# Kernel optimization log

Hardware: AMD Instinct MI355X
Metric: run time of the kernel (lower is better)

Reference implementation:

```python
import jax, jax.numpy as jnp
import numpy as np

D_MODEL = 1024
NUM_HEADS = 16
D_K = D_MODEL // NUM_HEADS


def setup_inputs() -> dict:
    key = jax.random.key(0)
    ks = jax.random.split(key, 11)
    B, T = 4, 2048
    s = 1.0 / np.sqrt(D_MODEL)
    inp = {
        'query': jax.random.normal(ks[0], (B, T, D_MODEL), jnp.float32),
        'key': jax.random.normal(ks[1], (B, T, D_MODEL), jnp.float32),
        'value': jax.random.normal(ks[2], (B, T, D_MODEL), jnp.float32),
        'Wq': jax.random.normal(ks[3], (D_MODEL, D_MODEL), jnp.float32) * s,
        'bq': jnp.zeros((D_MODEL,), jnp.float32),
        'Wk': jax.random.normal(ks[4], (D_MODEL, D_MODEL), jnp.float32) * s,
        'bk': jnp.zeros((D_MODEL,), jnp.float32),
        'Wv': jax.random.normal(ks[5], (D_MODEL, D_MODEL), jnp.float32) * s,
        'bv': jnp.zeros((D_MODEL,), jnp.float32),
        'Wo': jax.random.normal(ks[6], (D_MODEL, D_MODEL), jnp.float32) * s,
        'bo': jnp.zeros((D_MODEL,), jnp.float32),
    }
    return inp


def reference(query, key, value, Wq, bq, Wk, bk, Wv, bv, Wo, bo):
    B, Tq, _ = query.shape
    Tk = key.shape[1]
    # projections then split heads: [B,T,H,Dk] -> [B,H,T,Dk]
    Q = (query @ Wq + bq).reshape(B, Tq, NUM_HEADS, D_K).transpose(0, 2, 1, 3)
    K = (key @ Wk + bk).reshape(B, Tk, NUM_HEADS, D_K).transpose(0, 2, 1, 3)
    V = (value @ Wv + bv).reshape(B, Tk, NUM_HEADS, D_K).transpose(0, 2, 1, 3)
    scores = jnp.einsum('bhtd,bhsd->bhts', Q, K) / jnp.sqrt(jnp.float32(D_K))
    attn = jax.nn.softmax(scores, axis=-1)  # mask=None, dropout=0 (eval)
    ctx = jnp.einsum('bhts,bhsd->bhtd', attn, V)
    ctx = ctx.transpose(0, 2, 1, 3).reshape(B, Tq, D_MODEL)
    return ctx @ Wo + bo
```

## Files before the change

kernel.cpp:

```cpp
#include <hip/hip_runtime.h>
#include <hip/hip_bf16.h>
#include <stdint.h>

#define TSEQ 2048
#define NH   16
#define DKH  64
#define DM   1024

typedef __attribute__((ext_vector_type(8))) __bf16 bf16x8;
typedef __attribute__((ext_vector_type(4))) float floatx4;

#if __has_builtin(__builtin_amdgcn_exp2f)
#define EXP2F(x) __builtin_amdgcn_exp2f(x)
#else
#define EXP2F(x) exp2f(x)
#endif

__device__ __forceinline__ unsigned short f2bf(float f) {
  union { float f; unsigned u; } v; v.f = f;
  return (unsigned short)((v.u + 0x7fffu + ((v.u >> 16) & 1u)) >> 16);
}
__device__ __forceinline__ unsigned pack2bf(float a, float b) {
  float2 f; f.x = a; f.y = b;
  __hip_bfloat162 h = __float22bfloat162_rn(f);
  unsigned u; __builtin_memcpy(&u, &h, 4); return u;
}
__device__ __forceinline__ bf16x8 ld_frag(const unsigned short* p) {
  bf16x8 r; __builtin_memcpy(&r, p, 16); return r;
}
__device__ __forceinline__ void cp16(unsigned short* dst, const unsigned short* src) {
  uint4 t; __builtin_memcpy(&t, src, 16); __builtin_memcpy(dst, &t, 16);
}
__device__ __forceinline__ void cvt4(unsigned short* dst, const float* src) {
  float4 t; __builtin_memcpy(&t, src, 16);
  uint2 u; u.x = pack2bf(t.x, t.y); u.y = pack2bf(t.z, t.w);
  __builtin_memcpy(dst, &u, 8);
}

__global__ void wt_transpose(const float* __restrict__ in,
                             unsigned short* __restrict__ out) {
  __shared__ unsigned short tile[32][33];
  int bx = blockIdx.x * 32, by = blockIdx.y * 32;
  int x = threadIdx.x;
  for (int j = threadIdx.y; j < 32; j += 8)
    tile[j][x] = f2bf(in[(size_t)(by + j) * DM + bx + x]);
  __syncthreads();
  for (int j = threadIdx.y; j < 32; j += 8)
    out[(size_t)(bx + j) * DM + by + x] = tile[x][j];
}

template<int MODE>
__global__ __launch_bounds__(256, 2) void gemm_proj(
    const void* __restrict__ Araw,
    const unsigned short* __restrict__ WT,
    const float* __restrict__ bias,
    void* __restrict__ outraw) {
  const int LD = 40;
  __shared__ __align__(16) unsigned short Asm[128 * LD];
  __shared__ __align__(16) unsigned short Bsm[128 * LD];
  const int tid = threadIdx.x;
  const int wave = tid >> 6, lane = tid & 63;
  const int quad = lane >> 4, l16 = lane & 15;
  const int wm = wave & 1, wn = wave >> 1;
  const int m0 = blockIdx.y * 128, n0 = blockIdx.x * 128;

  floatx4 acc[4][4];
#pragma unroll
  for (int i = 0; i < 4; i++)
#pragma unroll
    for (int j = 0; j < 4; j++) acc[i][j] = (floatx4){0.f, 0.f, 0.f, 0.f};

  for (int k0 = 0; k0 < DM; k0 += 32) {
    if (MODE == 2) {
      const unsigned short* A16 = (const unsigned short*)Araw;
#pragma unroll
      for (int i = 0; i < 2; i++) {
        int c = tid + 256 * i;
        int row = c >> 2, k8 = (c & 3) * 8;
        cp16(&Asm[row * LD + k8], &A16[(size_t)(m0 + row) * DM + k0 + k8]);
      }
    } else {
      const float* A32 = (const float*)Araw;
#pragma unroll
      for (int i = 0; i < 4; i++) {
        int c = tid + 256 * i;
        int row = c >> 3, f4 = (c & 7) * 4;
        cvt4(&Asm[row * LD + f4], &A32[(size_t)(m0 + row) * DM + k0 + f4]);
      }
    }
#pragma unroll
    for (int i = 0; i < 2; i++) {
      int c = tid + 256 * i;
      int row = c >> 2, k8 = (c & 3) * 8;
      cp16(&Bsm[row * LD + k8], &WT[(size_t)(n0 + row) * DM + k0 + k8]);
    }
    __syncthreads();
    bf16x8 af[4], bfr[4];
#pragma unroll
    for (int mt = 0; mt < 4; mt++)
      af[mt] = ld_frag(&Asm[(wm * 64 + mt * 16 + l16) * LD + quad * 8]);
#pragma unroll
    for (int nt = 0; nt < 4; nt++)
      bfr[nt] = ld_frag(&Bsm[(wn * 64 + nt * 16 + l16) * LD + quad * 8]);
#pragma unroll
    for (int mt = 0; mt < 4; mt++)
#pragma unroll
      for (int nt = 0; nt < 4; nt++)
        acc[mt][nt] = __builtin_amdgcn_mfma_f32_16x16x32_bf16(af[mt], bfr[nt], acc[mt][nt], 0, 0, 0);
    __syncthreads();
  }

#pragma unroll
  for (int nt = 0; nt < 4; nt++) {
    int n = n0 + wn * 64 + nt * 16 + l16;
    float bv = bias[n];
#pragma unroll
    for (int mt = 0; mt < 4; mt++) {
#pragma unroll
      for (int r = 0; r < 4; r++) {
        int m = m0 + wm * 64 + mt * 16 + quad * 4 + r;
        float val = acc[mt][nt][r] + bv;
        if (MODE == 0) {
          int b = m >> 11, t = m & 2047, h = n >> 6, dk = n & 63;
          ((unsigned short*)outraw)[(size_t)(((b * NH + h) * TSEQ) + t) * DKH + dk] = f2bf(val);
        } else if (MODE == 1) {
          int b = m >> 11, t = m & 2047, h = n >> 6, dk = n & 63;
          ((unsigned short*)outraw)[(size_t)(((b * NH + h) * DKH) + dk) * TSEQ + t] = f2bf(val);
        } else {
          ((float*)outraw)[(size_t)m * DM + n] = val;
        }
      }
    }
  }
}

__global__ __launch_bounds__(256, 4) void flash_attn(
    const unsigned short* __restrict__ Q,
    const unsigned short* __restrict__ K,
    const unsigned short* __restrict__ VT,
    unsigned short* __restrict__ ctx) {
  const int LD = 72;
  __shared__ __align__(16) unsigned short QP[128 * LD];
  __shared__ __align__(16) unsigned short Ksm[64 * LD];
  __shared__ __align__(16) unsigned short Vsm[64 * LD];

  const int tid = threadIdx.x;
  const int wave = tid >> 6, lane = tid & 63;
  const int quad = lane >> 4, l16 = lane & 15;
  const int bh = blockIdx.y;
  const int t0 = blockIdx.x * 128;
  const unsigned short* Qg = Q + (size_t)bh * TSEQ * DKH;
  const unsigned short* Kg = K + (size_t)bh * TSEQ * DKH;
  const unsigned short* Vg = VT + (size_t)bh * DKH * TSEQ;

#pragma unroll
  for (int i = 0; i < 4; i++) {
    int c = tid + 256 * i;
    int row = c >> 3, k8 = (c & 7) * 8;
    cp16(&QP[row * LD + k8], &Qg[(size_t)(t0 + row) * DKH + k8]);
  }
  __syncthreads();
  bf16x8 qf[2][2];
#pragma unroll
  for (int qt = 0; qt < 2; qt++)
#pragma unroll
    for (int ks = 0; ks < 2; ks++)
      qf[qt][ks] = ld_frag(&QP[(wave * 32 + qt * 16 + l16) * LD + ks * 32 + quad * 8]);

  unsigned short* Pw = &QP[wave * 32 * LD];

  floatx4 O[2][4];
  float mrun[2], lrun[2];
#pragma unroll
  for (int qt = 0; qt < 2; qt++) {
#pragma unroll
    for (int dt = 0; dt < 4; dt++) O[qt][dt] = (floatx4){0.f, 0.f, 0.f, 0.f};
    mrun[qt] = -1e30f; lrun[qt] = 0.f;
  }
  const float sl = 0.125f * 1.44269504f;

  for (int j0 = 0; j0 < TSEQ; j0 += 64) {
#pragma unroll
    for (int i = 0; i < 2; i++) {
      int c = tid + 256 * i;
      int row = c >> 3, k8 = (c & 7) * 8;
      cp16(&Ksm[row * LD + k8], &Kg[(size_t)(j0 + row) * DKH + k8]);
      cp16(&Vsm[row * LD + k8], &Vg[(size_t)row * TSEQ + j0 + k8]);
    }
    __syncthreads();

    bf16x8 kf[4][2];
#pragma unroll
    for (int kt = 0; kt < 4; kt++)
#pragma unroll
      for (int ks = 0; ks < 2; ks++)
        kf[kt][ks] = ld_frag(&Ksm[(kt * 16 + l16) * LD + ks * 32 + quad * 8]);
    floatx4 st[4][2];
#pragma unroll
    for (int kt = 0; kt < 4; kt++)
#pragma unroll
      for (int qt = 0; qt < 2; qt++) {
        floatx4 a = (floatx4){0.f, 0.f, 0.f, 0.f};
        a = __builtin_amdgcn_mfma_f32_16x16x32_bf16(kf[kt][0], qf[qt][0], a, 0, 0, 0);
        a = __builtin_amdgcn_mfma_f32_16x16x32_bf16(kf[kt][1], qf[qt][1], a, 0, 0, 0);
        st[kt][qt] = a;
      }

    float aO[2][4];
#pragma unroll
    for (int qt = 0; qt < 2; qt++) {
      float mx = -3e38f;
#pragma unroll
      for (int kt = 0; kt < 4; kt++)
#pragma unroll
        for (int r = 0; r < 4; r++) mx = fmaxf(mx, st[kt][qt][r]);
      mx = fmaxf(mx, __shfl_xor(mx, 16, 64));
      mx = fmaxf(mx, __shfl_xor(mx, 32, 64));
      mx *= sl;
      float mnew = fmaxf(mrun[qt], mx);
      float alpha = EXP2F(mrun[qt] - mnew);
      mrun[qt] = mnew;
      float rs = 0.f;
#pragma unroll
      for (int kt = 0; kt < 4; kt++) {
        float p0 = EXP2F(st[kt][qt][0] * sl - mnew);
        float p1 = EXP2F(st[kt][qt][1] * sl - mnew);
        float p2 = EXP2F(st[kt][qt][2] * sl - mnew);
        float p3 = EXP2F(st[kt][qt][3] * sl - mnew);
        rs += (p0 + p1) + (p2 + p3);
        uint2 u; u.x = pack2bf(p0, p1); u.y = pack2bf(p2, p3);
        __builtin_memcpy(&Pw[(qt * 16 + l16) * LD + kt * 16 + quad * 4], &u, 8);
      }
      rs += __shfl_xor(rs, 16, 64);
      rs += __shfl_xor(rs, 32, 64);
      lrun[qt] = lrun[qt] * alpha + rs;
#pragma unroll
      for (int r = 0; r < 4; r++)
        aO[qt][r] = __shfl(alpha, quad * 20 + r, 64);
    }
    __syncthreads();

#pragma unroll
    for (int qt = 0; qt < 2; qt++)
#pragma unroll
      for (int dt = 0; dt < 4; dt++)
#pragma unroll
        for (int r = 0; r < 4; r++) O[qt][dt][r] *= aO[qt][r];

    bf16x8 vf[4][2];
#pragma unroll
    for (int dt = 0; dt < 4; dt++)
#pragma unroll
      for (int ks = 0; ks < 2; ks++)
        vf[dt][ks] = ld_frag(&Vsm[(dt * 16 + l16) * LD + ks * 32 + quad * 8]);
#pragma unroll
    for (int qt = 0; qt < 2; qt++) {
      bf16x8 pf[2];
#pragma unroll
      for (int ks = 0; ks < 2; ks++)
        pf[ks] = ld_frag(&Pw[(qt * 16 + l16) * LD + ks * 32 + quad * 8]);
#pragma unroll
      for (int dt = 0; dt < 4; dt++) {
        O[qt][dt] = __builtin_amdgcn_mfma_f32_16x16x32_bf16(pf[0], vf[dt][0], O[qt][dt], 0, 0, 0);
        O[qt][dt] = __builtin_amdgcn_mfma_f32_16x16x32_bf16(pf[1], vf[dt][1], O[qt][dt], 0, 0, 0);
      }
    }
    __syncthreads();
  }

  int b = bh >> 4, h = bh & 15;
#pragma unroll
  for (int qt = 0; qt < 2; qt++) {
#pragma unroll
    for (int r = 0; r < 4; r++) {
      float linv = 1.0f / __shfl(lrun[qt], quad * 20 + r, 64);
      int t = t0 + wave * 32 + qt * 16 + quad * 4 + r;
#pragma unroll
      for (int dt = 0; dt < 4; dt++) {
        int dk = dt * 16 + l16;
        ctx[((size_t)b * TSEQ + t) * DM + h * DKH + dk] = f2bf(O[qt][dt][r] * linv);
      }
    }
  }
}

extern "C" void kernel_launch(void* const* d_in, const int* in_sizes, int n_in,
                              void* d_out, int out_size, void* d_ws, size_t ws_size,
                              hipStream_t stream) {
  const float* q  = (const float*)d_in[0];
  const float* k  = (const float*)d_in[1];
  const float* v  = (const float*)d_in[2];
  const float* Wq = (const float*)d_in[3];
  const float* bq = (const float*)d_in[4];
  const float* Wk = (const float*)d_in[5];
  const float* bk = (const float*)d_in[6];
  const float* Wv = (const float*)d_in[7];
  const float* bv = (const float*)d_in[8];
  const float* Wo = (const float*)d_in[9];
  const float* bo = (const float*)d_in[10];

  const size_t MiB = 1024 * 1024;
  int nb;
  if      (ws_size >= 72 * MiB) nb = 4;
  else if (ws_size >= 40 * MiB) nb = 2;
  else                          nb = 1;
  const int passes = 4 / nb;

  unsigned char* ws = (unsigned char*)d_ws;
  unsigned short* WqT = (unsigned short*)(ws + 0 * MiB);
  unsigned short* WkT = (unsigned short*)(ws + 2 * MiB);
  unsigned short* WvT = (unsigned short*)(ws + 4 * MiB);
  unsigned short* WoT = (unsigned short*)(ws + 6 * MiB);
  const size_t tensorB = (size_t)nb * 4 * MiB;
  unsigned short* Qp = (unsigned short*)(ws + 8 * MiB);
  unsigned short* Kp = (unsigned short*)((unsigned char*)Qp + tensorB);
  unsigned short* Vp = (unsigned short*)((unsigned char*)Kp + tensorB);
  unsigned short* Cx = (unsigned short*)((unsigned char*)Vp + tensorB);

  dim3 tb(32, 8), tg(32, 32);
  wt_transpose<<<tg, tb, 0, stream>>>(Wq, WqT);
  wt_transpose<<<tg, tb, 0, stream>>>(Wk, WkT);
  wt_transpose<<<tg, tb, 0, stream>>>(Wv, WvT);
  wt_transpose<<<tg, tb, 0, stream>>>(Wo, WoT);

  const size_t passElems = (size_t)nb * TSEQ * DM;
  for (int p = 0; p < passes; p++) {
    const float* qp = q + (size_t)p * passElems;
    const float* kp = k + (size_t)p * passElems;
    const float* vp = v + (size_t)p * passElems;
    float* outp = (float*)d_out + (size_t)p * passElems;

    dim3 gg(8, nb * 16);
    gemm_proj<0><<<gg, 256, 0, stream>>>(qp, WqT, bq, Qp);
    gemm_proj<0><<<gg, 256, 0, stream>>>(kp, WkT, bk, Kp);
    gemm_proj<1><<<gg, 256, 0, stream>>>(vp, WvT, bv, Vp);

    flash_attn<<<dim3(16, nb * 16), 256, 0, stream>>>(Qp, Kp, Vp, Cx);

    gemm_proj<2><<<gg, 256, 0, stream>>>(Cx, WoT, bo, outp);
  }
}
```

Before: 444.1 us.

## Use direct global-to-LDS loads with XOR swizzle in GEMM and attention

Replaces register-staged global-to-shared copies in the projection GEMMs and flash attention with buffer global_load_lds 16-byte transfers into XOR-swizzled, unpadded LDS layouts. fp32 A tiles are now kept as fp32 in LDS and converted to bf16 when fragments are read, instead of at copy time. It also fuses the four weight-transpose launches into one, raises the GEMM occupancy hint, and drops one barrier in the attention loop. The aim is to cut VGPR traffic, LDS bank conflicts and launch overhead. The removed barrier depends on each wave's P region staying private, and the fp32 A tile doubles LDS use for that operand.

```diff
diff --git a/kernel.cpp b/kernel.cpp
--- a/kernel.cpp
+++ b/kernel.cpp
@@ -9,6 +9,8 @@
 
 typedef __attribute__((ext_vector_type(8))) __bf16 bf16x8;
 typedef __attribute__((ext_vector_type(4))) float floatx4;
+typedef __attribute__((address_space(1))) void gvoid_t;
+typedef __attribute__((address_space(3))) void lvoid_t;
 
 #if __has_builtin(__builtin_amdgcn_exp2f)
 #define EXP2F(x) __builtin_amdgcn_exp2f(x)
@@ -25,45 +27,100 @@
   __hip_bfloat162 h = __float22bfloat162_rn(f);
   unsigned u; __builtin_memcpy(&u, &h, 4); return u;
 }
-__device__ __forceinline__ bf16x8 ld_frag(const unsigned short* p) {
+__device__ __forceinline__ bf16x8 cvt8(float4 a, float4 b) {
+  unsigned u[4] = {pack2bf(a.x, a.y), pack2bf(a.z, a.w), pack2bf(b.x, b.y), pack2bf(b.z, b.w)};
+  bf16x8 r; __builtin_memcpy(&r, u, 16); return r;
+}
+__device__ __forceinline__ bf16x8 ld_frag(const void* p) {
   bf16x8 r; __builtin_memcpy(&r, p, 16); return r;
 }
-__device__ __forceinline__ void cp16(unsigned short* dst, const unsigned short* src) {
-  uint4 t; __builtin_memcpy(&t, src, 16); __builtin_memcpy(dst, &t, 16);
-}
-__device__ __forceinline__ void cvt4(unsigned short* dst, const float* src) {
-  float4 t; __builtin_memcpy(&t, src, 16);
-  uint2 u; u.x = pack2bf(t.x, t.y); u.y = pack2bf(t.z, t.w);
-  __builtin_memcpy(dst, &u, 8);
-}
-
-__global__ void wt_transpose(const float* __restrict__ in,
-                             unsigned short* __restrict__ out) {
+__device__ __forceinline__ void gl2lds16(const void* g, void* l) {
+  __builtin_amdgcn_global_load_lds((gvoid_t*)(uintptr_t)g,
+                                   (lvoid_t*)(unsigned)(uintptr_t)l, 16, 0, 0);
+}
+
+__global__ void wt_transpose4(const float* __restrict__ w0, const float* __restrict__ w1,
+                              const float* __restrict__ w2, const float* __restrict__ w3,
+                              unsigned short* __restrict__ out) {
   __shared__ unsigned short tile[32][33];
+  const float* srcs[4] = {w0, w1, w2, w3};
+  const float* in = srcs[blockIdx.z];
+  unsigned short* o = out + (size_t)blockIdx.z * DM * DM;
   int bx = blockIdx.x * 32, by = blockIdx.y * 32;
   int x = threadIdx.x;
   for (int j = threadIdx.y; j < 32; j += 8)
     tile[j][x] = f2bf(in[(size_t)(by + j) * DM + bx + x]);
   __syncthreads();
   for (int j = threadIdx.y; j < 32; j += 8)
-    out[(size_t)(bx + j) * DM + by + x] = tile[x][j];
+    o[(size_t)(bx + j) * DM + by + x] = tile[x][j];
 }
 
 template<int MODE>
-__global__ __launch_bounds__(256, 2) void gemm_proj(
+__global__ __launch_bounds__(256, 3) void gemm_proj(
     const void* __restrict__ Araw,
     const unsigned short* __restrict__ WT,
     const float* __restrict__ bias,
     void* __restrict__ outraw) {
-  const int LD = 40;
-  __shared__ __align__(16) unsigned short Asm[128 * LD];
-  __shared__ __align__(16) unsigned short Bsm[128 * LD];
+  constexpr int ABYTES = (MODE == 2) ? 8192 : 16384;
+  __shared__ __align__(16) unsigned char Asm[ABYTES];
+  __shared__ __align__(16) unsigned char Bsm[8192];
   const int tid = threadIdx.x;
   const int wave = tid >> 6, lane = tid & 63;
   const int quad = lane >> 4, l16 = lane & 15;
   const int wm = wave & 1, wn = wave >> 1;
   const int m0 = blockIdx.y * 128, n0 = blockIdx.x * 128;
 
+  const float* gA32[4];
+  const unsigned short* gA16[2];
+  const unsigned short* gB[2];
+  char *ldsA[4], *ldsB[2];
+  if (MODE != 2) {
+    const float* A32 = (const float*)Araw;
+#pragma unroll
+    for (int it = 0; it < 4; it++) {
+      int cl = (wave * 4 + it) * 64 + lane;
+      int row = cl >> 3, phys = cl & 7;
+      int cG = phys ^ (row & 7);
+      gA32[it] = A32 + (size_t)(m0 + row) * DM + cG * 4;
+      ldsA[it] = (char*)Asm + (wave * 4 + it) * 1024;
+    }
+  } else {
+    const unsigned short* A16 = (const unsigned short*)Araw;
+#pragma unroll
+    for (int it = 0; it < 2; it++) {
+      int cl = (wave * 2 + it) * 64 + lane;
+      int row = cl >> 2, phys = cl & 3;
+      int cG = phys ^ ((row >> 1) & 3);
+      gA16[it] = A16 + (size_t)(m0 + row) * DM + cG * 8;
+      ldsA[it] = (char*)Asm + (wave * 2 + it) * 1024;
+    }
+  }
+#pragma unroll
+  for (int it = 0; it < 2; it++) {
+    int cl = (wave * 2 + it) * 64 + lane;
+    int row = cl >> 2, phys = cl & 3;
+    int cG = phys ^ ((row >> 1) & 3);
+    gB[it] = WT + (size_t)(n0 + row) * DM + cG * 8;
+    ldsB[it] = (char*)Bsm + (wave * 2 + it) * 1024;
+  }
+
+  int offA0[4], offA1[4], offB[4];
+#pragma unroll
+  for (int mt = 0; mt < 4; mt++) {
+    int row = wm * 64 + mt * 16 + l16;
+    if (MODE != 2) {
+      offA0[mt] = row * 128 + ((2 * quad) ^ (row & 7)) * 16;
+      offA1[mt] = row * 128 + ((2 * quad + 1) ^ (row & 7)) * 16;
+    } else {
+      offA0[mt] = row * 64 + (quad ^ ((row >> 1) & 3)) * 16;
+    }
+  }
+#pragma unroll
+  for (int nt = 0; nt < 4; nt++) {
+    int row = wn * 64 + nt * 16 + l16;
+    offB[nt] = row * 64 + (quad ^ ((row >> 1) & 3)) * 16;
+  }
+
   floatx4 acc[4][4];
 #pragma unroll
   for (int i = 0; i < 4; i++)
@@ -71,37 +128,32 @@
     for (int j = 0; j < 4; j++) acc[i][j] = (floatx4){0.f, 0.f, 0.f, 0.f};
 
   for (int k0 = 0; k0 < DM; k0 += 32) {
-    if (MODE == 2) {
-      const unsigned short* A16 = (const unsigned short*)Araw;
-#pragma unroll
-      for (int i = 0; i < 2; i++) {
-        int c = tid + 256 * i;
-        int row = c >> 2, k8 = (c & 3) * 8;
-        cp16(&Asm[row * LD + k8], &A16[(size_t)(m0 + row) * DM + k0 + k8]);
-      }
+    if (MODE != 2) {
+#pragma unroll
+      for (int it = 0; it < 4; it++) { gl2lds16(gA32[it], ldsA[it]); gA32[it] += 32; }
     } else {
-      const float* A32 = (const float*)Araw;
-#pragma unroll
-      for (int i = 0; i < 4; i++) {
-        int c = tid + 256 * i;
-        int row = c >> 3, f4 = (c & 7) * 4;
-        cvt4(&Asm[row * LD + f4], &A32[(size_t)(m0 + row) * DM + k0 + f4]);
-      }
-    }
-#pragma unroll
-    for (int i = 0; i < 2; i++) {
-      int c = tid + 256 * i;
-      int row = c >> 2, k8 = (c & 3) * 8;
-      cp16(&Bsm[row * LD + k8], &WT[(size_t)(n0 + row) * DM + k0 + k8]);
-    }
+#pragma unroll
+      for (int it = 0; it < 2; it++) { gl2lds16(gA16[it], ldsA[it]); gA16[it] += 32; }
+    }
+#pragma unroll
+    for (int it = 0; it < 2; it++) { gl2lds16(gB[it], ldsB[it]); gB[it] += 32; }
     __syncthreads();
+
     bf16x8 af[4], bfr[4];
 #pragma unroll
-    for (int mt = 0; mt < 4; mt++)
-      af[mt] = ld_frag(&Asm[(wm * 64 + mt * 16 + l16) * LD + quad * 8]);
+    for (int mt = 0; mt < 4; mt++) {
+      if (MODE != 2) {
+        float4 fa, fb;
+        __builtin_memcpy(&fa, Asm + offA0[mt], 16);
+        __builtin_memcpy(&fb, Asm + offA1[mt], 16);
+        af[mt] = cvt8(fa, fb);
+      } else {
+        af[mt] = ld_frag(Asm + offA0[mt]);
+      }
+    }
 #pragma unroll
     for (int nt = 0; nt < 4; nt++)
-      bfr[nt] = ld_frag(&Bsm[(wn * 64 + nt * 16 + l16) * LD + quad * 8]);
+      bfr[nt] = ld_frag(Bsm + offB[nt]);
 #pragma unroll
     for (int mt = 0; mt < 4; mt++)
 #pragma unroll
@@ -139,10 +191,9 @@
     const unsigned short* __restrict__ K,
     const unsigned short* __restrict__ VT,
     unsigned short* __restrict__ ctx) {
-  const int LD = 72;
-  __shared__ __align__(16) unsigned short QP[128 * LD];
-  __shared__ __align__(16) unsigned short Ksm[64 * LD];
-  __shared__ __align__(16) unsigned short Vsm[64 * LD];
+  __shared__ __align__(16) unsigned short QP[128 * 64];
+  __shared__ __align__(16) unsigned short Ksm[64 * 64];
+  __shared__ __align__(16) unsigned short Vsm[64 * 64];
 
   const int tid = threadIdx.x;
   const int wave = tid >> 6, lane = tid & 63;
@@ -154,20 +205,41 @@
   const unsigned short* Vg = VT + (size_t)bh * DKH * TSEQ;
 
 #pragma unroll
-  for (int i = 0; i < 4; i++) {
-    int c = tid + 256 * i;
-    int row = c >> 3, k8 = (c & 7) * 8;
-    cp16(&QP[row * LD + k8], &Qg[(size_t)(t0 + row) * DKH + k8]);
+  for (int it = 0; it < 4; it++) {
+    int cl = (wave * 4 + it) * 64 + lane;
+    int row = cl >> 3, phys = cl & 7;
+    int cG = phys ^ (row & 7);
+    gl2lds16(Qg + (size_t)(t0 + row) * DKH + cG * 8, (char*)QP + (wave * 4 + it) * 1024);
+  }
+  const unsigned short* gK[2];
+  const unsigned short* gV[2];
+  char *ldsK[2], *ldsV[2];
+#pragma unroll
+  for (int it = 0; it < 2; it++) {
+    int cl = (wave * 2 + it) * 64 + lane;
+    int row = cl >> 3, phys = cl & 7;
+    int cG = phys ^ (row & 7);
+    gK[it] = Kg + (size_t)row * DKH + cG * 8;
+    gV[it] = Vg + (size_t)row * TSEQ + cG * 8;
+    ldsK[it] = (char*)Ksm + (wave * 2 + it) * 1024;
+    ldsV[it] = (char*)Vsm + (wave * 2 + it) * 1024;
   }
   __syncthreads();
+
+  const int sw = l16 & 7;
+  int foff[2];
+#pragma unroll
+  for (int ks = 0; ks < 2; ks++)
+    foff[ks] = l16 * 128 + ((ks * 4 + quad) ^ sw) * 16;
+
   bf16x8 qf[2][2];
 #pragma unroll
   for (int qt = 0; qt < 2; qt++)
 #pragma unroll
     for (int ks = 0; ks < 2; ks++)
-      qf[qt][ks] = ld_frag(&QP[(wave * 32 + qt * 16 + l16) * LD + ks * 32 + quad * 8]);
-
-  unsigned short* Pw = &QP[wave * 32 * LD];
+      qf[qt][ks] = ld_frag((char*)QP + (wave * 32 + qt * 16) * 128 + foff[ks]);
+
+  char* Pw = (char*)QP + wave * 4096;
 
   floatx4 O[2][4];
   float mrun[2], lrun[2];
@@ -181,11 +253,9 @@
 
   for (int j0 = 0; j0 < TSEQ; j0 += 64) {
 #pragma unroll
-    for (int i = 0; i < 2; i++) {
-      int c = tid + 256 * i;
-      int row = c >> 3, k8 = (c & 7) * 8;
-      cp16(&Ksm[row * LD + k8], &Kg[(size_t)(j0 + row) * DKH + k8]);
-      cp16(&Vsm[row * LD + k8], &Vg[(size_t)row * TSEQ + j0 + k8]);
+    for (int it = 0; it < 2; it++) {
+      gl2lds16(gK[it], ldsK[it]); gK[it] += 64 * DKH;
+      gl2lds16(gV[it], ldsV[it]); gV[it] += 64;
     }
     __syncthreads();
 
@@ -194,7 +264,7 @@
     for (int kt = 0; kt < 4; kt++)
 #pragma unroll
       for (int ks = 0; ks < 2; ks++)
-        kf[kt][ks] = ld_frag(&Ksm[(kt * 16 + l16) * LD + ks * 32 + quad * 8]);
+        kf[kt][ks] = ld_frag((char*)Ksm + kt * 16 * 128 + foff[ks]);
     floatx4 st[4][2];
 #pragma unroll
     for (int kt = 0; kt < 4; kt++)
@@ -229,7 +299,8 @@
         float p3 = EXP2F(st[kt][qt][3] * sl - mnew);
         rs += (p0 + p1) + (p2 + p3);
         uint2 u; u.x = pack2bf(p0, p1); u.y = pack2bf(p2, p3);
-        __builtin_memcpy(&Pw[(qt * 16 + l16) * LD + kt * 16 + quad * 4], &u, 8);
+        int physC = (2 * kt + (quad >> 1)) ^ sw;
+        __builtin_memcpy(Pw + (qt * 16 + l16) * 128 + physC * 16 + (quad & 1) * 8, &u, 8);
       }
       rs += __shfl_xor(rs, 16, 64);
       rs += __shfl_xor(rs, 32, 64);
@@ -238,7 +309,6 @@
       for (int r = 0; r < 4; r++)
         aO[qt][r] = __shfl(alpha, quad * 20 + r, 64);
     }
-    __syncthreads();
 
 #pragma unroll
     for (int qt = 0; qt < 2; qt++)
@@ -252,13 +322,13 @@
     for (int dt = 0; dt < 4; dt++)
 #pragma unroll
       for (int ks = 0; ks < 2; ks++)
-        vf[dt][ks] = ld_frag(&Vsm[(dt * 16 + l16) * LD + ks * 32 + quad * 8]);
+        vf[dt][ks] = ld_frag((char*)Vsm + dt * 16 * 128 + foff[ks]);
 #pragma unroll
     for (int qt = 0; qt < 2; qt++) {
       bf16x8 pf[2];
 #pragma unroll
       for (int ks = 0; ks < 2; ks++)
-        pf[ks] = ld_frag(&Pw[(qt * 16 + l16) * LD + ks * 32 + quad * 8]);
+        pf[ks] = ld_frag(Pw + qt * 16 * 128 + foff[ks]);
 #pragma unroll
       for (int dt = 0; dt < 4; dt++) {
         O[qt][dt] = __builtin_amdgcn_mfma_f32_16x16x32_bf16(pf[0], vf[dt][0], O[qt][dt], 0, 0, 0);
@@ -307,21 +377,18 @@
   const int passes = 4 / nb;
 
   unsigned char* ws = (unsigned char*)d_ws;
-  unsigned short* WqT = (unsigned short*)(ws + 0 * MiB);
-  unsigned short* WkT = (unsigned short*)(ws + 2 * MiB);
-  unsigned short* WvT = (unsigned short*)(ws + 4 * MiB);
-  unsigned short* WoT = (unsigned short*)(ws + 6 * MiB);
+  unsigned short* WTs = (unsigned short*)ws;
+  unsigned short* WqT = WTs + 0 * DM * DM;
+  unsigned short* WkT = WTs + 1 * DM * DM;
+  unsigned short* WvT = WTs + 2 * DM * DM;
+  unsigned short* WoT = WTs + 3 * DM * DM;
   const size_t tensorB = (size_t)nb * 4 * MiB;
   unsigned short* Qp = (unsigned short*)(ws + 8 * MiB);
   unsigned short* Kp = (unsigned short*)((unsigned char*)Qp + tensorB);
   unsigned short* Vp = (unsigned short*)((unsigned char*)Kp + tensorB);
   unsigned short* Cx = (unsigned short*)((unsigned char*)Vp + tensorB);
 
-  dim3 tb(32, 8), tg(32, 32);
-  wt_transpose<<<tg, tb, 0, stream>>>(Wq, WqT);
-  wt_transpose<<<tg, tb, 0, stream>>>(Wk, WkT);
-  wt_transpose<<<tg, tb, 0, stream>>>(Wv, WvT);
-  wt_transpose<<<tg, tb, 0, stream>>>(Wo, WoT);
+  wt_transpose4<<<dim3(32, 32, 4), dim3(32, 8), 0, stream>>>(Wq, Wk, Wv, Wo, WTs);
 
   const size_t passElems = (size_t)nb * TSEQ * DM;
   for (int p = 0; p < passes; p++) {
```

Result: faster. 435.1 us (-2.0%).
